# Kernel tuning notes

Measured on AMD Instinct MI355X. Metric: run time of the kernel, lower is better.

The kernel has to match this reference:

```python
import jax, jax.numpy as jnp
import numpy as np

N = 100000      # total nodes in batched graph
E = 3200000     # total edges (avg degree 32)
G = 128         # number of graphs in batch
F_IN = 512      # raw node feature dim
NC = 128        # num_classes = projected feature dim (GraphConv layer-0 input)
HID = 256       # hid_channels
OUT = 10        # out_channels
LYR = 3         # args.lyr
EPS = 1e-5      # BatchNorm1d eps


def setup_inputs() -> dict:
    key = jax.random.key(0)
    ks = jax.random.split(key, 20)
    h = jax.random.normal(ks[0], (N, F_IN), dtype=jnp.float32)
    src = jax.random.randint(ks[1], (E,), 0, N, dtype=jnp.int32)
    dst = jax.random.randint(ks[2], (E,), 0, N, dtype=jnp.int32)
    # contiguous sorted graph assignment: every graph non-empty
    graph_ids = (jnp.arange(N, dtype=jnp.int32) * G) // N
    w_init = jax.random.normal(ks[3], (NC, F_IN), dtype=jnp.float32) * 0.05
    inp = dict(h=h, src=src, dst=dst, graph_ids=graph_ids, w_init=w_init)
    dims = [NC, HID, HID]
    for i in range(LYR):
        inp[f"lw{i}"] = jax.random.normal(ks[4 + i], (dims[i], HID), dtype=jnp.float32) * 0.05
        inp[f"lb{i}"] = jnp.zeros((HID,), jnp.float32)
        inp[f"gamma{i}"] = jnp.ones((HID,), jnp.float32)
        inp[f"beta{i}"] = jnp.zeros((HID,), jnp.float32)
    inp["fc_w"] = jax.random.normal(ks[10], (HID, OUT), dtype=jnp.float32) * 0.05
    inp["fc_b"] = jnp.zeros((OUT,), jnp.float32)
    return inp


def _forward(h, src, dst, graph_ids, w_init, layers, fc_w, fc_b):
    # symmetric normalization (DGL GraphConv norm='both')
    ones_e = jnp.ones((E,), h.dtype)
    out_deg = jax.ops.segment_sum(ones_e, src, num_segments=N)
    in_deg = jax.ops.segment_sum(ones_e, dst, num_segments=N)
    norm_src = jnp.where(out_deg > 0, out_deg ** -0.5, 0.0)  # [N]
    norm_dst = jnp.where(in_deg > 0, in_deg ** -0.5, 0.0)    # [N]

    h = h @ w_init.T  # [N, NC]
    for (lw, lb, gamma, beta) in layers:
        # GraphConv: (D_out^-1/2) gather -> scatter-sum -> (D_in^-1/2), then linear
        m = (h * norm_src[:, None])[src]                       # [E, d]
        agg = jax.ops.segment_sum(m, dst, num_segments=N)       # [N, d]
        h = (agg * norm_dst[:, None]) @ lw + lb                 # [N, HID]
        # BatchNorm1d (training-mode batch stats, biased variance) + ReLU
        mu = jnp.mean(h, axis=0)
        var = jnp.mean((h - mu) ** 2, axis=0)
        h = jax.nn.relu((h - mu) * jax.lax.rsqrt(var + EPS) * gamma + beta)
    # dgl.max_nodes: per-graph max over nodes
    hg = jax.ops.segment_max(h, graph_ids, num_segments=G)      # [G, HID]
    return hg @ fc_w + fc_b                                     # [G, OUT]


def reference(h, src, dst, graph_ids, w_init,
              lw0, lb0, gamma0, beta0,
              lw1, lb1, gamma1, beta1,
              lw2, lb2, gamma2, beta2,
              fc_w, fc_b):
    layers = [(lw0, lb0, gamma0, beta0),
              (lw1, lb1, gamma1, beta1),
              (lw2, lb2, gamma2, beta2)]
    return _forward(h, src, dst, graph_ids, w_init, layers, fc_w, fc_b)
```

## Files before the change

### kernel.cpp

```cpp
#include <hip/hip_runtime.h>
#include <hip/hip_bf16.h>

#define N_NODES 100000
#define N_EDGES 3200000
#define N_GRAPHS 128
#define FIN 512
#define NCLS 128
#define HID 256
#define OUT_DIM 10
#define BN_EPS 1e-5f

#define NBUCK 391
#define EPB   ((N_EDGES + NBUCK - 1) / NBUCK)

typedef unsigned short ush;
typedef ush su16x8 __attribute__((ext_vector_type(8)));
typedef ush su16x4 __attribute__((ext_vector_type(4)));
typedef __bf16 bf16x8v __attribute__((ext_vector_type(8)));
typedef float f32x4v __attribute__((ext_vector_type(4)));

__device__ __forceinline__ float bf2f(ush u) {
    union { unsigned int i; float f; } v; v.i = ((unsigned int)u) << 16; return v.f;
}
__device__ __forceinline__ ush f2bf(float f) {
    union { float f; unsigned int i; } v; v.f = f;
    unsigned int r = v.i + 0x7FFFu + ((v.i >> 16) & 1u);
    return (ush)(r >> 16);
}

template <typename T>
__device__ __forceinline__ auto mfma_sel(T a, T b, f32x4v c, int)
    -> decltype(__builtin_amdgcn_mfma_f32_16x16x32_bf16(a, b, c, 0, 0, 0)) {
    return __builtin_amdgcn_mfma_f32_16x16x32_bf16(a, b, c, 0, 0, 0);
}
template <typename T>
__device__ __forceinline__ f32x4v mfma_sel(T a, T b, f32x4v c, long) {
    return __builtin_amdgcn_mfma_f32_16x16x32_bf16(
        __builtin_bit_cast(bf16x8v, a), __builtin_bit_cast(bf16x8v, b), c, 0, 0, 0);
}
__device__ __forceinline__ f32x4v MFMA_BF16(su16x8 a, su16x8 b, f32x4v c) {
    return mfma_sel(a, b, c, 0);
}

__global__ void odeg_kernel(const int* __restrict__ src, int* __restrict__ odeg) {
    int e = blockIdx.x * 256 + threadIdx.x;
    if (e < N_EDGES) atomicAdd(&odeg[src[e]], 1);
}
__global__ void nsrc_kernel(const int* __restrict__ odeg, float* __restrict__ nsrc) {
    int n = blockIdx.x * 256 + threadIdx.x;
    if (n < N_NODES) {
        int od = odeg[n];
        nsrc[n] = od > 0 ? rsqrtf((float)od) : 0.f;
    }
}

__global__ __launch_bounds__(256) void histA_kernel(const int* __restrict__ dst,
                                                    int* __restrict__ hist) {
    __shared__ int hc[NBUCK];
    int tid = threadIdx.x, blk = blockIdx.x;
    for (int i = tid; i < NBUCK; i += 256) hc[i] = 0;
    __syncthreads();
    int e0 = blk * EPB, e1 = e0 + EPB; if (e1 > N_EDGES) e1 = N_EDGES;
    for (int e = e0 + tid; e < e1; e += 256) atomicAdd(&hc[dst[e] >> 8], 1);
    __syncthreads();
    for (int i = tid; i < NBUCK; i += 256) hist[(size_t)blk * NBUCK + i] = hc[i];
}

__global__ __launch_bounds__(512) void bcnt_kernel(const int* __restrict__ hist,
                                                   int* __restrict__ bcnt) {
    __shared__ int ws[8];
    int b = blockIdx.x, tid = threadIdx.x;
    int lane = tid & 63, wid = tid >> 6;
    int v = (tid < NBUCK) ? hist[(size_t)tid * NBUCK + b] : 0;
    #pragma unroll
    for (int off = 32; off > 0; off >>= 1) v += __shfl_down(v, off, 64);
    if (lane == 0) ws[wid] = v;
    __syncthreads();
    if (tid == 0) {
        int s = 0;
        #pragma unroll
        for (int w = 0; w < 8; w++) s += ws[w];
        bcnt[b] = s;
    }
}

__global__ __launch_bounds__(512) void bscan_kernel(const int* __restrict__ bcnt,
                                                    int* __restrict__ bbase) {
    __shared__ int a[512];
    int tid = threadIdx.x;
    int v = (tid < NBUCK) ? bcnt[tid] : 0;
    a[tid] = v;
    __syncthreads();
    for (int s = 1; s < 512; s <<= 1) {
        int y = (tid >= s) ? a[tid - s] : 0;
        __syncthreads();
        a[tid] += y;
        __syncthreads();
    }
    if (tid < NBUCK) bbase[tid] = a[tid] - v;
    if (tid == 0) bbase[NBUCK] = N_EDGES;
}

__global__ __launch_bounds__(512) void boff_kernel(const int* __restrict__ hist,
                                                   const int* __restrict__ bbase,
                                                   int* __restrict__ off) {
    __shared__ int a[512];
    int b = blockIdx.x, tid = threadIdx.x;
    int v = (tid < NBUCK) ? hist[(size_t)tid * NBUCK + b] : 0;
    a[tid] = v;
    __syncthreads();
    for (int s = 1; s < 512; s <<= 1) {
        int y = (tid >= s) ? a[tid - s] : 0;
        __syncthreads();
        a[tid] += y;
        __syncthreads();
    }
    if (tid < NBUCK) off[(size_t)tid * NBUCK + b] = bbase[b] + a[tid] - v;
}

__global__ __launch_bounds__(256) void stage_kernel(const int* __restrict__ src,
                                                    const int* __restrict__ dst,
                                                    const int* __restrict__ off,
                                                    unsigned int* __restrict__ staged) {
    __shared__ int cur[NBUCK];
    int tid = threadIdx.x, blk = blockIdx.x;
    for (int i = tid; i < NBUCK; i += 256) cur[i] = off[(size_t)blk * NBUCK + i];
    __syncthreads();
    int e0 = blk * EPB, e1 = e0 + EPB; if (e1 > N_EDGES) e1 = N_EDGES;
    for (int e = e0 + tid; e < e1; e += 256) {
        int d = dst[e], s = src[e];
        int pos = atomicAdd(&cur[d >> 8], 1);
        staged[pos] = ((unsigned int)(d & 255) << 24) | (unsigned int)s;
    }
}

__global__ __launch_bounds__(256) void csr_kernel(const unsigned int* __restrict__ staged,
                                                  const int* __restrict__ bbase,
                                                  int* __restrict__ roff,
                                                  float* __restrict__ ndst,
                                                  int* __restrict__ csr) {
    __shared__ int cnt[256], pfx[256], cur[256];
    int b = blockIdx.x, tid = threadIdx.x;
    int beg = bbase[b], end = bbase[b + 1];
    int nodeBase = b * 256;
    int nNodes = N_NODES - nodeBase; if (nNodes > 256) nNodes = 256;
    cnt[tid] = 0;
    __syncthreads();
    for (int e = beg + tid; e < end; e += 256) atomicAdd(&cnt[staged[e] >> 24], 1);
    __syncthreads();
    int v = cnt[tid];
    pfx[tid] = v;
    __syncthreads();
    for (int s = 1; s < 256; s <<= 1) {
        int y = (tid >= s) ? pfx[tid - s] : 0;
        __syncthreads();
        pfx[tid] += y;
        __syncthreads();
    }
    int excl = pfx[tid] - v;
    pfx[tid] = excl;
    cur[tid] = 0;
    if (tid < nNodes) {
        int node = nodeBase + tid;
        roff[node] = beg + excl;
        ndst[node] = v > 0 ? rsqrtf((float)v) : 0.f;
    }
    if (b == NBUCK - 1 && tid == 0) roff[N_NODES] = N_EDGES;
    __syncthreads();
    for (int e = beg + tid; e < end; e += 256) {
        unsigned int w = staged[e];
        int dl = w >> 24;
        int pos = beg + pfx[dl] + atomicAdd(&cur[dl], 1);
        csr[pos] = (int)(w & 0xFFFFFFu);
    }
}

__global__ void cvt_w0_kernel(const float* __restrict__ w, ush* __restrict__ o) {
    int i = blockIdx.x * 256 + threadIdx.x;
    if (i < NCLS * FIN) o[i] = f2bf(w[i]);
}
__global__ void cvt_lwT_kernel(const float* __restrict__ lw, ush* __restrict__ o, int K) {
    int i = blockIdx.x * 256 + threadIdx.x;
    if (i < K * HID) {
        int n = i / K, k = i % K;
        o[i] = f2bf(lw[(size_t)k * HID + n]);
    }
}

template <bool A_F32, bool DO_STATS>
__global__ __launch_bounds__(256) void mfma_gemm(
    const void* __restrict__ Aptr, const ush* __restrict__ BT,
    ush* __restrict__ C, int M, int K, int NN,
    const float* __restrict__ rowscale, const float* __restrict__ bias,
    float* __restrict__ stats)
{
    __shared__ __align__(16) ush As[128][40];
    __shared__ __align__(16) ush Bs[128][40];
    const int bn0 = blockIdx.x * 128;
    const int bm0 = blockIdx.y * 128;
    const int tid = threadIdx.x;
    const int lane = tid & 63;
    const int wv = tid >> 6;
    const int wm = (wv >> 1) * 64;
    const int wn = (wv & 1) * 64;
    const int lm = lane & 15;
    const int lg = lane >> 4;

    f32x4v zero = {0.f, 0.f, 0.f, 0.f};
    f32x4v acc[4][4];
    #pragma unroll
    for (int mi = 0; mi < 4; mi++)
        #pragma unroll
        for (int ni = 0; ni < 4; ni++) acc[mi][ni] = zero;

    for (int k0 = 0; k0 < K; k0 += 32) {
        #pragma unroll
        for (int i = 0; i < 2; i++) {
            int seg = tid + i * 256;
            int n = seg >> 2, kp = seg & 3;
            su16x8 v = *(const su16x8*)&BT[(size_t)(bn0 + n) * K + k0 + kp * 8];
            *(su16x8*)&Bs[n][kp * 8] = v;
        }
        if constexpr (A_F32) {
            const float* Af = (const float*)Aptr;
            #pragma unroll
            for (int i = 0; i < 4; i++) {
                int seg = tid + i * 256;
                int m = seg >> 3, kp = seg & 7;
                int gm = bm0 + m; if (gm >= M) gm = M - 1;
                float4 v = *(const float4*)&Af[(size_t)gm * K + k0 + kp * 4];
                su16x4 o = { f2bf(v.x), f2bf(v.y), f2bf(v.z), f2bf(v.w) };
                *(su16x4*)&As[m][kp * 4] = o;
            }
        } else {
            const ush* Ab = (const ush*)Aptr;
            #pragma unroll
            for (int i = 0; i < 2; i++) {
                int seg = tid + i * 256;
                int m = seg >> 2, kp = seg & 3;
                int gm = bm0 + m; if (gm >= M) gm = M - 1;
                su16x8 v = *(const su16x8*)&Ab[(size_t)gm * K + k0 + kp * 8];
                *(su16x8*)&As[m][kp * 8] = v;
            }
        }
        __syncthreads();
        su16x8 af[4], bfr[4];
        #pragma unroll
        for (int i = 0; i < 4; i++)
            af[i] = *(const su16x8*)&As[wm + i * 16 + lm][lg * 8];
        #pragma unroll
        for (int i = 0; i < 4; i++)
            bfr[i] = *(const su16x8*)&Bs[wn + i * 16 + lm][lg * 8];
        #pragma unroll
        for (int mi = 0; mi < 4; mi++)
            #pragma unroll
            for (int ni = 0; ni < 4; ni++)
                acc[mi][ni] = MFMA_BF16(af[mi], bfr[ni], acc[mi][ni]);
        __syncthreads();
    }

    float s4[4] = {0.f, 0.f, 0.f, 0.f}, q4[4] = {0.f, 0.f, 0.f, 0.f};
    #pragma unroll
    for (int mi = 0; mi < 4; mi++) {
        #pragma unroll
        for (int j = 0; j < 4; j++) {
            int gm = bm0 + wm + mi * 16 + lg * 4 + j;
            bool valid = gm < M;
            float rs = (rowscale && valid) ? rowscale[gm] : 1.f;
            #pragma unroll
            for (int ni = 0; ni < 4; ni++) {
                int gn = bn0 + wn + ni * 16 + lm;
                float v = acc[mi][ni][j] * rs;
                if (bias) v += bias[gn];
                if (valid) {
                    C[(size_t)gm * NN + gn] = f2bf(v);
                    if constexpr (DO_STATS) { s4[ni] += v; q4[ni] += v * v; }
                }
            }
        }
    }
    if constexpr (DO_STATS) {
        #pragma unroll
        for (int ni = 0; ni < 4; ni++) {
            s4[ni] += __shfl_xor(s4[ni], 16); s4[ni] += __shfl_xor(s4[ni], 32);
            q4[ni] += __shfl_xor(q4[ni], 16); q4[ni] += __shfl_xor(q4[ni], 32);
        }
        if (lg == 0) {
            #pragma unroll
            for (int ni = 0; ni < 4; ni++) {
                int gn = bn0 + wn + ni * 16 + lm;
                atomicAdd(&stats[gn], s4[ni]);
                atomicAdd(&stats[HID + gn], q4[ni]);
            }
        }
    }
}

__global__ __launch_bounds__(256) void agg128(const ush* __restrict__ hs,
                                              const int* __restrict__ roff,
                                              const int* __restrict__ csr,
                                              ush* __restrict__ out)
{
    int node = (blockIdx.x * 256 + threadIdx.x) >> 6;
    int lane = threadIdx.x & 63;
    if (node >= N_NODES) return;
    int q = lane >> 4;
    int c0 = (lane & 15) * 8;
    int beg = roff[node], end = roff[node + 1];
    float acc[8] = {};
    for (int e = beg + q; e < end; e += 4) {
        int s = csr[e];
        su16x8 v = *(const su16x8*)&hs[(size_t)s * 128 + c0];
        #pragma unroll
        for (int j = 0; j < 8; j++) acc[j] += bf2f(v[j]);
    }
    #pragma unroll
    for (int j = 0; j < 8; j++) {
        acc[j] += __shfl_xor(acc[j], 16);
        acc[j] += __shfl_xor(acc[j], 32);
    }
    if (lane < 16) {
        su16x8 o;
        #pragma unroll
        for (int j = 0; j < 8; j++) o[j] = f2bf(acc[j]);
        *(su16x8*)&out[(size_t)node * 128 + c0] = o;
    }
}

__global__ __launch_bounds__(256) void agg256_bn(const ush* __restrict__ pre,
                                                 const float* __restrict__ bnab,
                                                 const float* __restrict__ nsrc,
                                                 const int* __restrict__ roff,
                                                 const int* __restrict__ csr,
                                                 ush* __restrict__ out)
{
    int node = (blockIdx.x * 256 + threadIdx.x) >> 6;
    int lane = threadIdx.x & 63;
    if (node >= N_NODES) return;
    int half = lane >> 5;
    int c0 = (lane & 31) * 8;
    float a[8], b[8];
    #pragma unroll
    for (int j = 0; j < 8; j++) { a[j] = bnab[c0 + j]; b[j] = bnab[HID + c0 + j]; }
    int beg = roff[node], end = roff[node + 1];
    float acc[8] = {};
    for (int e = beg + half; e < end; e += 2) {
        int s = csr[e];
        float ns = nsrc[s];
        su16x8 v = *(const su16x8*)&pre[(size_t)s * 256 + c0];
        #pragma unroll
        for (int j = 0; j < 8; j++) {
            float x = fmaxf(fmaf(bf2f(v[j]), a[j], b[j]), 0.f);
            acc[j] = fmaf(x, ns, acc[j]);
        }
    }
    #pragma unroll
    for (int j = 0; j < 8; j++) acc[j] += __shfl_xor(acc[j], 32);
    if (lane < 32) {
        su16x8 o;
        #pragma unroll
        for (int j = 0; j < 8; j++) o[j] = f2bf(acc[j]);
        *(su16x8*)&out[(size_t)node * 256 + c0] = o;
    }
}

__global__ void bnprep_kernel(const float* __restrict__ stats,
                              const float* __restrict__ gamma, const float* __restrict__ beta,
                              float* __restrict__ ab) {
    int c = threadIdx.x;
    const float inv_n = 1.f / (float)N_NODES;
    float mu = stats[c] * inv_n;
    float var = fmaf(-mu, mu, stats[HID + c] * inv_n);
    float a = gamma[c] * rsqrtf(var + BN_EPS);
    ab[c] = a;
    ab[HID + c] = fmaf(-mu, a, beta[c]);
}

__global__ void gstart_kernel(const int* __restrict__ gids, int* __restrict__ gstart) {
    int n = blockIdx.x * 256 + threadIdx.x;
    if (n >= N_NODES) return;
    int g = gids[n];
    int gp = (n == 0) ? -1 : gids[n - 1];
    for (int gg = gp + 1; gg <= g; gg++) gstart[gg] = n;
    if (n == N_NODES - 1) {
        for (int gg = g + 1; gg <= N_GRAPHS; gg++) gstart[gg] = N_NODES;
    }
}

__global__ void segmax_bn(const ush* __restrict__ pre, const float* __restrict__ bnab,
                          const int* __restrict__ gstart, float* __restrict__ hg) {
    int g = blockIdx.x;
    int chunk = blockIdx.y;
    int c = threadIdx.x;
    float a = bnab[c], b = bnab[HID + c];
    int beg = gstart[g], end = gstart[g + 1];
    int len = end - beg;
    int per = (len + 7) >> 3;
    int s = beg + chunk * per;
    int e = s + per; if (e > end) e = end;
    float m = 0.f;
    for (int n = s; n < e; n++)
        m = fmaxf(m, fmaf(bf2f(pre[(size_t)n * HID + c]), a, b));
    m = fmaxf(m, 0.f);
    atomicMax((int*)&hg[g * HID + c], __float_as_int(m));
}

__global__ void fc_kernel(const float* __restrict__ hg, const float* __restrict__ w,
                          const float* __restrict__ b, float* __restrict__ out) {
    int idx = blockIdx.x * 256 + threadIdx.x;
    if (idx >= N_GRAPHS * OUT_DIM) return;
    int g = idx / OUT_DIM, j = idx % OUT_DIM;
    float s = b[j];
    for (int c = 0; c < HID; c++) s += hg[g * HID + c] * w[c * OUT_DIM + j];
    out[idx] = s;
}

extern "C" void kernel_launch(void* const* d_in, const int* in_sizes, int n_in,
                              void* d_out, int out_size, void* d_ws, size_t ws_size,
                              hipStream_t stream) {
    const float* h      = (const float*)d_in[0];
    const int*   src    = (const int*)d_in[1];
    const int*   dst    = (const int*)d_in[2];
    const int*   gids   = (const int*)d_in[3];
    const float* w_init = (const float*)d_in[4];
    const float* lw[3]    = { (const float*)d_in[5],  (const float*)d_in[9],  (const float*)d_in[13] };
    const float* lb[3]    = { (const float*)d_in[6],  (const float*)d_in[10], (const float*)d_in[14] };
    const float* gamma[3] = { (const float*)d_in[7],  (const float*)d_in[11], (const float*)d_in[15] };
    const float* beta[3]  = { (const float*)d_in[8],  (const float*)d_in[12], (const float*)d_in[16] };
    const float* fc_w = (const float*)d_in[17];
    const float* fc_b = (const float*)d_in[18];
    float* out = (float*)d_out;

    char* ws = (char*)d_ws;
    size_t off_b = 0;
    auto alloc = [&](size_t bytes) { size_t o = off_b; off_b += (bytes + 255) & ~(size_t)255; return o; };
    size_t o_h0s   = alloc((size_t)N_NODES * NCLS * 2);
    size_t o_aggb  = alloc((size_t)N_NODES * HID * 2);
    size_t o_P0    = alloc((size_t)N_NODES * HID * 2);
    size_t o_P1    = alloc((size_t)N_NODES * HID * 2);
    size_t o_wB0   = alloc((size_t)NCLS * FIN * 2);
    size_t o_lwT0  = alloc((size_t)HID * NCLS * 2);
    size_t o_lwT1  = alloc((size_t)HID * HID * 2);
    size_t o_lwT2  = alloc((size_t)HID * HID * 2);
    size_t o_nsrc  = alloc((size_t)N_NODES * 4);
    size_t o_ndst  = alloc((size_t)N_NODES * 4);
    size_t o_odeg  = alloc((size_t)N_NODES * 4);
    size_t o_roff  = alloc((size_t)(N_NODES + 1) * 4);
    size_t o_csr   = alloc((size_t)N_EDGES * 4);
    size_t o_stg   = alloc((size_t)N_EDGES * 4);
    size_t o_hist  = alloc((size_t)NBUCK * NBUCK * 4);
    size_t o_off   = alloc((size_t)NBUCK * NBUCK * 4);
    size_t o_bcnt  = alloc((size_t)(NBUCK + 1) * 4);
    size_t o_bbase = alloc((size_t)(NBUCK + 1) * 4);
    size_t o_stats = alloc((size_t)3 * 2 * HID * 4);
    size_t o_bnab  = alloc((size_t)3 * 2 * HID * 4);
    size_t o_gst   = alloc((size_t)(N_GRAPHS + 1) * 4);
    size_t o_hg    = alloc((size_t)N_GRAPHS * HID * 4);
    if (off_b > ws_size) return;

    ush*   h0s  = (ush*)(ws + o_h0s);
    ush*   aggb = (ush*)(ws + o_aggb);
    ush*   P[2] = { (ush*)(ws + o_P0), (ush*)(ws + o_P1) };
    ush*   wB0  = (ush*)(ws + o_wB0);
    ush*   lwT[3] = { (ush*)(ws + o_lwT0), (ush*)(ws + o_lwT1), (ush*)(ws + o_lwT2) };
    float* nsrc = (float*)(ws + o_nsrc);
    float* ndst = (float*)(ws + o_ndst);
    int*   odeg = (int*)(ws + o_odeg);
    int*   roff = (int*)(ws + o_roff);
    int*   csr  = (int*)(ws + o_csr);
    unsigned int* stg = (unsigned int*)(ws + o_stg);
    int*   hist = (int*)(ws + o_hist);
    int*   boff = (int*)(ws + o_off);
    int*   bcnt = (int*)(ws + o_bcnt);
    int*   bbase= (int*)(ws + o_bbase);
    float* stats= (float*)(ws + o_stats);
    float* bnab = (float*)(ws + o_bnab);
    int*   gst  = (int*)(ws + o_gst);
    float* hg   = (float*)(ws + o_hg);

    const int eb = (N_EDGES + 255) / 256;
    const int nb = (N_NODES + 255) / 256;

    hipMemsetAsync(odeg, 0, (size_t)N_NODES * 4, stream);
    hipMemsetAsync(stats, 0, 3 * 2 * HID * 4, stream);
    hipMemsetAsync(hg, 0, (size_t)N_GRAPHS * HID * 4, stream);

    odeg_kernel<<<eb, 256, 0, stream>>>(src, odeg);
    nsrc_kernel<<<nb, 256, 0, stream>>>(odeg, nsrc);

    histA_kernel<<<NBUCK, 256, 0, stream>>>(dst, hist);
    bcnt_kernel<<<NBUCK, 512, 0, stream>>>(hist, bcnt);
    bscan_kernel<<<1, 512, 0, stream>>>(bcnt, bbase);
    boff_kernel<<<NBUCK, 512, 0, stream>>>(hist, bbase, boff);
    stage_kernel<<<NBUCK, 256, 0, stream>>>(src, dst, boff, stg);
    csr_kernel<<<NBUCK, 256, 0, stream>>>(stg, bbase, roff, ndst, csr);

    gstart_kernel<<<nb, 256, 0, stream>>>(gids, gst);

    cvt_w0_kernel<<<(NCLS * FIN + 255) / 256, 256, 0, stream>>>(w_init, wB0);
    cvt_lwT_kernel<<<(NCLS * HID + 255) / 256, 256, 0, stream>>>(lw[0], lwT[0], NCLS);
    cvt_lwT_kernel<<<(HID * HID + 255) / 256, 256, 0, stream>>>(lw[1], lwT[1], HID);
    cvt_lwT_kernel<<<(HID * HID + 255) / 256, 256, 0, stream>>>(lw[2], lwT[2], HID);

    const int mblocks = (N_NODES + 127) / 128;
    const int aggblocks = (N_NODES * 64 + 255) / 256;

    {
        dim3 grid(NCLS / 128, mblocks);
        mfma_gemm<true, false><<<grid, 256, 0, stream>>>(h, wB0, h0s, N_NODES, FIN, NCLS,
                                                         nsrc, nullptr, nullptr);
    }

    agg128<<<aggblocks, 256, 0, stream>>>(h0s, roff, csr, aggb);
    {
        dim3 grid(HID / 128, mblocks);
        mfma_gemm<false, true><<<grid, 256, 0, stream>>>(aggb, lwT[0], P[0], N_NODES, NCLS, HID,
                                                         ndst, lb[0], stats);
    }
    bnprep_kernel<<<1, 256, 0, stream>>>(stats, gamma[0], beta[0], bnab);

    for (int l = 1; l < 3; l++) {
        ush* pin  = P[(l + 1) & 1];
        ush* pout = P[l & 1];
        agg256_bn<<<aggblocks, 256, 0, stream>>>(pin, bnab + (l - 1) * 2 * HID, nsrc,
                                                 roff, csr, aggb);
        dim3 grid(HID / 128, mblocks);
        mfma_gemm<false, true><<<grid, 256, 0, stream>>>(aggb, lwT[l], pout, N_NODES, HID, HID,
                                                         ndst, lb[l], stats + l * 2 * HID);
        bnprep_kernel<<<1, 256, 0, stream>>>(stats + l * 2 * HID, gamma[l], beta[l],
                                             bnab + l * 2 * HID);
    }

    {
        dim3 grid(N_GRAPHS, 8);
        segmax_bn<<<grid, 256, 0, stream>>>(P[0], bnab + 2 * 2 * HID, gst, hg);
    }
    fc_kernel<<<(N_GRAPHS * OUT_DIM + 255) / 256, 256, 0, stream>>>(hg, fc_w, fc_b, out);
}
```

Measured before the change: 1.160 ms.

## Precompute BN+ReLU+norm per node before aggregation, privatize degree counters, unroll gathers

BatchNorm, ReLU and source-norm scaling move out of the per-edge gather into a separate per-node pass (bnq_kernel) that writes a normalized bf16 buffer Q. The aggregation kernels then only sum gathered rows, with two accumulators and nontemporal loads and stores. This removes the per-edge FMAs and the nsrc gathers (E-scale work) at the cost of one extra N×256 read-write pass. Out-degree atomics are split across 8 privatized copies to reduce contention, the bnprep launches are folded into the consumer kernels, and segmax is unrolled by two.

```diff
diff --git a/kernel.cpp b/kernel.cpp
--- a/kernel.cpp
+++ b/kernel.cpp
@@ -42,14 +42,17 @@
     return mfma_sel(a, b, c, 0);
 }
 
-__global__ void odeg_kernel(const int* __restrict__ src, int* __restrict__ odeg) {
+__global__ void odeg_kernel(const int* __restrict__ src, int* __restrict__ odeg8) {
     int e = blockIdx.x * 256 + threadIdx.x;
-    if (e < N_EDGES) atomicAdd(&odeg[src[e]], 1);
-}
-__global__ void nsrc_kernel(const int* __restrict__ odeg, float* __restrict__ nsrc) {
+    int c = blockIdx.x & 7;
+    if (e < N_EDGES) atomicAdd(&odeg8[(size_t)c * N_NODES + src[e]], 1);
+}
+__global__ void nsrc_kernel(const int* __restrict__ odeg8, float* __restrict__ nsrc) {
     int n = blockIdx.x * 256 + threadIdx.x;
     if (n < N_NODES) {
-        int od = odeg[n];
+        int od = 0;
+        #pragma unroll
+        for (int c = 0; c < 8; c++) od += odeg8[(size_t)c * N_NODES + n];
         nsrc[n] = od > 0 ? rsqrtf((float)od) : 0.f;
     }
 }
@@ -307,73 +310,107 @@
     int q = lane >> 4;
     int c0 = (lane & 15) * 8;
     int beg = roff[node], end = roff[node + 1];
-    float acc[8] = {};
-    for (int e = beg + q; e < end; e += 4) {
-        int s = csr[e];
-        su16x8 v = *(const su16x8*)&hs[(size_t)s * 128 + c0];
-        #pragma unroll
-        for (int j = 0; j < 8; j++) acc[j] += bf2f(v[j]);
+    float accA[8] = {}, accB[8] = {};
+    int e = beg + q;
+    for (; e + 4 < end; e += 8) {
+        int s0 = __builtin_nontemporal_load(&csr[e]);
+        int s1 = __builtin_nontemporal_load(&csr[e + 4]);
+        su16x8 v0 = *(const su16x8*)&hs[(size_t)s0 * 128 + c0];
+        su16x8 v1 = *(const su16x8*)&hs[(size_t)s1 * 128 + c0];
+        #pragma unroll
+        for (int j = 0; j < 8; j++) { accA[j] += bf2f(v0[j]); accB[j] += bf2f(v1[j]); }
+    }
+    if (e < end) {
+        int s0 = __builtin_nontemporal_load(&csr[e]);
+        su16x8 v0 = *(const su16x8*)&hs[(size_t)s0 * 128 + c0];
+        #pragma unroll
+        for (int j = 0; j < 8; j++) accA[j] += bf2f(v0[j]);
     }
     #pragma unroll
     for (int j = 0; j < 8; j++) {
-        acc[j] += __shfl_xor(acc[j], 16);
-        acc[j] += __shfl_xor(acc[j], 32);
+        accA[j] += accB[j];
+        accA[j] += __shfl_xor(accA[j], 16);
+        accA[j] += __shfl_xor(accA[j], 32);
     }
     if (lane < 16) {
         su16x8 o;
         #pragma unroll
-        for (int j = 0; j < 8; j++) o[j] = f2bf(acc[j]);
-        *(su16x8*)&out[(size_t)node * 128 + c0] = o;
-    }
-}
-
-__global__ __launch_bounds__(256) void agg256_bn(const ush* __restrict__ pre,
-                                                 const float* __restrict__ bnab,
-                                                 const float* __restrict__ nsrc,
-                                                 const int* __restrict__ roff,
-                                                 const int* __restrict__ csr,
-                                                 ush* __restrict__ out)
+        for (int j = 0; j < 8; j++) o[j] = f2bf(accA[j]);
+        __builtin_nontemporal_store(o, (su16x8*)&out[(size_t)node * 128 + c0]);
+    }
+}
+
+__global__ __launch_bounds__(256) void agg256(const ush* __restrict__ Q,
+                                              const int* __restrict__ roff,
+                                              const int* __restrict__ csr,
+                                              ush* __restrict__ out)
 {
     int node = (blockIdx.x * 256 + threadIdx.x) >> 6;
     int lane = threadIdx.x & 63;
     if (node >= N_NODES) return;
     int half = lane >> 5;
     int c0 = (lane & 31) * 8;
-    float a[8], b[8];
+    int beg = roff[node], end = roff[node + 1];
+    float accA[8] = {}, accB[8] = {};
+    int e = beg + half;
+    for (; e + 2 < end; e += 4) {
+        int s0 = __builtin_nontemporal_load(&csr[e]);
+        int s1 = __builtin_nontemporal_load(&csr[e + 2]);
+        su16x8 v0 = *(const su16x8*)&Q[(size_t)s0 * 256 + c0];
+        su16x8 v1 = *(const su16x8*)&Q[(size_t)s1 * 256 + c0];
+        #pragma unroll
+        for (int j = 0; j < 8; j++) { accA[j] += bf2f(v0[j]); accB[j] += bf2f(v1[j]); }
+    }
+    if (e < end) {
+        int s0 = __builtin_nontemporal_load(&csr[e]);
+        su16x8 v0 = *(const su16x8*)&Q[(size_t)s0 * 256 + c0];
+        #pragma unroll
+        for (int j = 0; j < 8; j++) accA[j] += bf2f(v0[j]);
+    }
     #pragma unroll
-    for (int j = 0; j < 8; j++) { a[j] = bnab[c0 + j]; b[j] = bnab[HID + c0 + j]; }
-    int beg = roff[node], end = roff[node + 1];
-    float acc[8] = {};
-    for (int e = beg + half; e < end; e += 2) {
-        int s = csr[e];
-        float ns = nsrc[s];
-        su16x8 v = *(const su16x8*)&pre[(size_t)s * 256 + c0];
-        #pragma unroll
-        for (int j = 0; j < 8; j++) {
-            float x = fmaxf(fmaf(bf2f(v[j]), a[j], b[j]), 0.f);
-            acc[j] = fmaf(x, ns, acc[j]);
-        }
-    }
-    #pragma unroll
-    for (int j = 0; j < 8; j++) acc[j] += __shfl_xor(acc[j], 32);
+    for (int j = 0; j < 8; j++) {
+        accA[j] += accB[j];
+        accA[j] += __shfl_xor(accA[j], 32);
+    }
     if (lane < 32) {
         su16x8 o;
         #pragma unroll
-        for (int j = 0; j < 8; j++) o[j] = f2bf(acc[j]);
-        *(su16x8*)&out[(size_t)node * 256 + c0] = o;
-    }
-}
-
-__global__ void bnprep_kernel(const float* __restrict__ stats,
-                              const float* __restrict__ gamma, const float* __restrict__ beta,
-                              float* __restrict__ ab) {
-    int c = threadIdx.x;
-    const float inv_n = 1.f / (float)N_NODES;
-    float mu = stats[c] * inv_n;
-    float var = fmaf(-mu, mu, stats[HID + c] * inv_n);
-    float a = gamma[c] * rsqrtf(var + BN_EPS);
-    ab[c] = a;
-    ab[HID + c] = fmaf(-mu, a, beta[c]);
+        for (int j = 0; j < 8; j++) o[j] = f2bf(accA[j]);
+        __builtin_nontemporal_store(o, (su16x8*)&out[(size_t)node * 256 + c0]);
+    }
+}
+
+__global__ __launch_bounds__(256) void bnq_kernel(const ush* __restrict__ P,
+                                                  const float* __restrict__ stats,
+                                                  const float* __restrict__ gamma,
+                                                  const float* __restrict__ beta,
+                                                  const float* __restrict__ nsrc,
+                                                  ush* __restrict__ Q)
+{
+    __shared__ float sa[HID], sb[HID];
+    int tid = threadIdx.x;
+    {
+        const float inv_n = 1.f / (float)N_NODES;
+        float mu = stats[tid] * inv_n;
+        float var = fmaf(-mu, mu, stats[HID + tid] * inv_n);
+        float a = gamma[tid] * rsqrtf(var + BN_EPS);
+        sa[tid] = a;
+        sb[tid] = fmaf(-mu, a, beta[tid]);
+    }
+    __syncthreads();
+    const int total = N_NODES * 32;
+    for (int idx = blockIdx.x * 256 + tid; idx < total; idx += gridDim.x * 256) {
+        int r = idx >> 5, c0 = (idx & 31) * 8;
+        su16x8 v = __builtin_nontemporal_load((const su16x8*)&P[(size_t)r * HID + c0]);
+        float ns = nsrc[r];
+        su16x8 o;
+        #pragma unroll
+        for (int j = 0; j < 8; j++) {
+            float x = fmaxf(fmaf(bf2f(v[j]), sa[c0 + j], sb[c0 + j]), 0.f) * ns;
+            o[j] = f2bf(x);
+        }
+        *(su16x8*)&Q[(size_t)r * HID + c0] = o;
+    }
 }
 
 __global__ void gstart_kernel(const int* __restrict__ gids, int* __restrict__ gstart) {
@@ -387,21 +424,33 @@
     }
 }
 
-__global__ void segmax_bn(const ush* __restrict__ pre, const float* __restrict__ bnab,
-                          const int* __restrict__ gstart, float* __restrict__ hg) {
+__global__ __launch_bounds__(256) void segmax_ab(const ush* __restrict__ pre,
+                                                 const float* __restrict__ stats,
+                                                 const float* __restrict__ gamma,
+                                                 const float* __restrict__ beta,
+                                                 const int* __restrict__ gstart,
+                                                 float* __restrict__ hg) {
+    int c = threadIdx.x;
+    const float inv_n = 1.f / (float)N_NODES;
+    float mu = stats[c] * inv_n;
+    float var = fmaf(-mu, mu, stats[HID + c] * inv_n);
+    float a = gamma[c] * rsqrtf(var + BN_EPS);
+    float b = fmaf(-mu, a, beta[c]);
     int g = blockIdx.x;
     int chunk = blockIdx.y;
-    int c = threadIdx.x;
-    float a = bnab[c], b = bnab[HID + c];
     int beg = gstart[g], end = gstart[g + 1];
     int len = end - beg;
     int per = (len + 7) >> 3;
     int s = beg + chunk * per;
     int e = s + per; if (e > end) e = end;
-    float m = 0.f;
-    for (int n = s; n < e; n++)
-        m = fmaxf(m, fmaf(bf2f(pre[(size_t)n * HID + c]), a, b));
-    m = fmaxf(m, 0.f);
+    float m0 = 0.f, m1 = 0.f;
+    int n = s;
+    for (; n + 1 < e; n += 2) {
+        m0 = fmaxf(m0, fmaf(bf2f(pre[(size_t)n * HID + c]), a, b));
+        m1 = fmaxf(m1, fmaf(bf2f(pre[(size_t)(n + 1) * HID + c]), a, b));
+    }
+    if (n < e) m0 = fmaxf(m0, fmaf(bf2f(pre[(size_t)n * HID + c]), a, b));
+    float m = fmaxf(fmaxf(m0, m1), 0.f);
     atomicMax((int*)&hg[g * HID + c], __float_as_int(m));
 }
 
@@ -436,15 +485,15 @@
     auto alloc = [&](size_t bytes) { size_t o = off_b; off_b += (bytes + 255) & ~(size_t)255; return o; };
     size_t o_h0s   = alloc((size_t)N_NODES * NCLS * 2);
     size_t o_aggb  = alloc((size_t)N_NODES * HID * 2);
-    size_t o_P0    = alloc((size_t)N_NODES * HID * 2);
-    size_t o_P1    = alloc((size_t)N_NODES * HID * 2);
+    size_t o_P     = alloc((size_t)N_NODES * HID * 2);
+    size_t o_Q     = alloc((size_t)N_NODES * HID * 2);
     size_t o_wB0   = alloc((size_t)NCLS * FIN * 2);
     size_t o_lwT0  = alloc((size_t)HID * NCLS * 2);
     size_t o_lwT1  = alloc((size_t)HID * HID * 2);
     size_t o_lwT2  = alloc((size_t)HID * HID * 2);
     size_t o_nsrc  = alloc((size_t)N_NODES * 4);
     size_t o_ndst  = alloc((size_t)N_NODES * 4);
-    size_t o_odeg  = alloc((size_t)N_NODES * 4);
+    size_t o_odeg8 = alloc((size_t)8 * N_NODES * 4);
     size_t o_roff  = alloc((size_t)(N_NODES + 1) * 4);
     size_t o_csr   = alloc((size_t)N_EDGES * 4);
     size_t o_stg   = alloc((size_t)N_EDGES * 4);
@@ -453,19 +502,19 @@
     size_t o_bcnt  = alloc((size_t)(NBUCK + 1) * 4);
     size_t o_bbase = alloc((size_t)(NBUCK + 1) * 4);
     size_t o_stats = alloc((size_t)3 * 2 * HID * 4);
-    size_t o_bnab  = alloc((size_t)3 * 2 * HID * 4);
     size_t o_gst   = alloc((size_t)(N_GRAPHS + 1) * 4);
     size_t o_hg    = alloc((size_t)N_GRAPHS * HID * 4);
     if (off_b > ws_size) return;
 
     ush*   h0s  = (ush*)(ws + o_h0s);
     ush*   aggb = (ush*)(ws + o_aggb);
-    ush*   P[2] = { (ush*)(ws + o_P0), (ush*)(ws + o_P1) };
+    ush*   P    = (ush*)(ws + o_P);
+    ush*   Q    = (ush*)(ws + o_Q);
     ush*   wB0  = (ush*)(ws + o_wB0);
     ush*   lwT[3] = { (ush*)(ws + o_lwT0), (ush*)(ws + o_lwT1), (ush*)(ws + o_lwT2) };
     float* nsrc = (float*)(ws + o_nsrc);
     float* ndst = (float*)(ws + o_ndst);
-    int*   odeg = (int*)(ws + o_odeg);
+    int*   odeg8= (int*)(ws + o_odeg8);
     int*   roff = (int*)(ws + o_roff);
     int*   csr  = (int*)(ws + o_csr);
     unsigned int* stg = (unsigned int*)(ws + o_stg);
@@ -474,19 +523,18 @@
     int*   bcnt = (int*)(ws + o_bcnt);
     int*   bbase= (int*)(ws + o_bbase);
     float* stats= (float*)(ws + o_stats);
-    float* bnab = (float*)(ws + o_bnab);
     int*   gst  = (int*)(ws + o_gst);
     float* hg   = (float*)(ws + o_hg);
 
     const int eb = (N_EDGES + 255) / 256;
     const int nb = (N_NODES + 255) / 256;
 
-    hipMemsetAsync(odeg, 0, (size_t)N_NODES * 4, stream);
+    hipMemsetAsync(odeg8, 0, (size_t)8 * N_NODES * 4, stream);
     hipMemsetAsync(stats, 0, 3 * 2 * HID * 4, stream);
     hipMemsetAsync(hg, 0, (size_t)N_GRAPHS * HID * 4, stream);
 
-    odeg_kernel<<<eb, 256, 0, stream>>>(src, odeg);
-    nsrc_kernel<<<nb, 256, 0, stream>>>(odeg, nsrc);
+    odeg_kernel<<<eb, 256, 0, stream>>>(src, odeg8);
+    nsrc_kernel<<<nb, 256, 0, stream>>>(odeg8, nsrc);
 
     histA_kernel<<<NBUCK, 256, 0, stream>>>(dst, hist);
     bcnt_kernel<<<NBUCK, 512, 0, stream>>>(hist, bcnt);
@@ -514,26 +562,22 @@
     agg128<<<aggblocks, 256, 0, stream>>>(h0s, roff, csr, aggb);
     {
         dim3 grid(HID / 128, mblocks);
-        mfma_gemm<false, true><<<grid, 256, 0, stream>>>(aggb, lwT[0], P[0], N_NODES, NCLS, HID,
+        mfma_gemm<false, true><<<grid, 256, 0, stream>>>(aggb, lwT[0], P, N_NODES, NCLS, HID,
                                                          ndst, lb[0], stats);
     }
-    bnprep_kernel<<<1, 256, 0, stream>>>(stats, gamma[0], beta[0], bnab);
 
     for (int l = 1; l < 3; l++) {
-        ush* pin  = P[(l + 1) & 1];
-        ush* pout = P[l & 1];
-        agg256_bn<<<aggblocks, 256, 0, stream>>>(pin, bnab + (l - 1) * 2 * HID, nsrc,
-                                                 roff, csr, aggb);
+        bnq_kernel<<<1024, 256, 0, stream>>>(P, stats + (l - 1) * 2 * HID,
+                                             gamma[l - 1], beta[l - 1], nsrc, Q);
+        agg256<<<aggblocks, 256, 0, stream>>>(Q, roff, csr, aggb);
         dim3 grid(HID / 128, mblocks);
-        mfma_gemm<false, true><<<grid, 256, 0, stream>>>(aggb, lwT[l], pout, N_NODES, HID, HID,
+        mfma_gemm<false, true><<<grid, 256, 0, stream>>>(aggb, lwT[l], P, N_NODES, HID, HID,
                                                          ndst, lb[l], stats + l * 2 * HID);
-        bnprep_kernel<<<1, 256, 0, stream>>>(stats + l * 2 * HID, gamma[l], beta[l],
-                                             bnab + l * 2 * HID);
     }
 
     {
         dim3 grid(N_GRAPHS, 8);
-        segmax_bn<<<grid, 256, 0, stream>>>(P[0], bnab + 2 * 2 * HID, gst, hg);
+        segmax_ab<<<grid, 256, 0, stream>>>(P, stats + 2 * 2 * HID, gamma[2], beta[2], gst, hg);
     }
     fc_kernel<<<(N_GRAPHS * OUT_DIM + 255) / 256, 256, 0, stream>>>(hg, fc_w, fc_b, out);
 }
```

After: 1.174 ms. About the same (+1.3%).
